# Kernel tuning notes

Measured on AMD Instinct MI355X. Metric: run time of the kernel, lower is better.

The kernel has to match this reference:

```python
import jax, jax.numpy as jnp
import numpy as np

# Constants from retinanet.settings (repo defaults, undefined in snippet; fixed here)
ALPHA = 0.95
GAMMA = 2.0
DAMPENING = 0.7           # DAMPENING_PARAMETER; gt_map simplified to all-False
MAX_POS_DIST = 30.0       # MAX_ANOT_ANCHOR_POSITION_DISTANCE
MAX_ANG_DIST = 20.0       # MAX_ANOT_ANCHOR_ANGLE_DISTANCE
EPS = 1e-4


def setup_inputs() -> dict:
    key = jax.random.key(0)
    k1, k2, k3, k4, k5 = jax.random.split(key, 5)
    B, N, K, C = 4, 300000, 64, 4
    classifications = jax.random.uniform(k1, (B, N, C), jnp.float32, 0.01, 0.99)
    regressions = jax.random.normal(k2, (B, N, 3), jnp.float32) * 5.0
    anchors = jax.random.uniform(k3, (B, N, 3), jnp.float32) * jnp.array([512.0, 512.0, 180.0])
    ann_xy_a = jax.random.uniform(k4, (B, K, 3), jnp.float32) * jnp.array([512.0, 512.0, 180.0])
    ann_cls = jax.random.randint(k5, (B, K, 1), 0, C).astype(jnp.float32)
    annotations = jnp.concatenate([ann_xy_a, ann_cls], axis=-1)  # [B,K,4]
    return {"classifications": classifications, "regressions": regressions,
            "anchors": anchors, "annotations": annotations}


def _per_image(classification, regression, ann, anchor):
    C = classification.shape[1]
    cls = jnp.clip(classification, EPS, 1.0 - EPS)
    # NxK broadcast distance matrices (the tile/transpose chain in the original)
    dx = jnp.abs(anchor[:, 0, None] - ann[None, :, 0])
    dy = jnp.abs(anchor[:, 1, None] - ann[None, :, 1])
    dalpha = jnp.abs(anchor[:, 2, None] - ann[None, :, 2])
    dxy = jnp.sqrt(dx * dx + dy * dy)                         # [N,K]
    dxy_min = jnp.min(dxy, axis=1)                            # [N]
    dxy_argmin = jnp.argmin(dxy, axis=1)                      # [N]
    a = jnp.take_along_axis(dalpha, dxy_argmin[:, None], axis=1)[:, 0]
    # target assignment
    neg = (dxy_min >= 1.5 * MAX_POS_DIST) | (a >= 1.5 * MAX_ANG_DIST)
    pos = (dxy_min < MAX_POS_DIST) & (a < MAX_ANG_DIST)
    assigned = ann[dxy_argmin]                                # [N,4] gather
    targets = jnp.full(cls.shape, -1.0, cls.dtype)
    targets = jnp.where(neg[:, None], 0.0, targets)
    targets = jnp.where(pos[:, None], 0.0, targets)
    onehot = jax.nn.one_hot(assigned[:, 3].astype(jnp.int32), C, dtype=cls.dtype)
    targets = jnp.where(pos[:, None] & (onehot > 0), 1.0, targets)
    num_pos = jnp.sum(pos).astype(cls.dtype)
    denom = jnp.maximum(num_pos, 1.0)
    # focal-weighted BCE
    alpha_factor = jnp.where(targets == 1.0, ALPHA, 1.0 - ALPHA)
    focal_weight = alpha_factor * jnp.where(targets == 1.0, 1.0 - cls, cls) ** GAMMA
    bce = -(targets * jnp.log(cls) + (1.0 - targets) * jnp.log(1.0 - cls))
    cls_loss = jnp.where(targets != -1.0, focal_weight * bce, 0.0) * DAMPENING
    cls_total = jnp.sum(cls_loss) / denom
    t = assigned[:, :3] - anchor
    diff_xy = jnp.abs(t[:, :2] - regression[:, :2])
    loss_xy = jnp.where(diff_xy <= 1.0 / 9.0, 0.5 * 9.0 * diff_xy ** 2, diff_xy - 0.5 / 9.0) * DAMPENING
    diff_ang = jnp.maximum((jnp.abs(t[:, 2] - regression[:, 2]) - 10.0) / 5.0, 0.0) * DAMPENING
    has_pos = num_pos > 0
    xy_mean = jnp.where(has_pos, jnp.sum(loss_xy * pos[:, None]) / (2.0 * denom), 0.0)
    ang_mean = jnp.where(has_pos, jnp.sum(diff_ang * pos) / denom, 0.0)
    return cls_total, xy_mean, ang_mean


def reference(classifications, regressions, anchors, annotations):
    anchor = anchors[0]  # original uses anchors[0,:,:] for all batch elements
    cls_l, xy_l, ang_l = jax.vmap(lambda c, r, an: _per_image(c, r, an, anchor))(
        classifications, regressions, annotations)
    return jnp.stack([jnp.mean(cls_l), jnp.mean(xy_l), jnp.mean(ang_l)])
```

## Files before the change

### kernel.cpp

```cpp
#include <hip/hip_runtime.h>
#include <cmath>

constexpr int Bk = 4;
constexpr int Nk = 300000;
constexpr int Kk = 64;
constexpr int BLOCK = 256;
constexpr int CHUNK = 4;
constexpr int SUPER = BLOCK * CHUNK;
constexpr int PBI = (Nk + SUPER - 1) / SUPER;
constexpr int NBLK = Bk * PBI;

#define C_ALPHA 0.95f
#define C_DAMP 0.7f


__global__ __launch_bounds__(BLOCK) void focal_main(
    const float* __restrict__ cls_,
    const float* __restrict__ reg_,
    const float* __restrict__ anc_,
    const float* __restrict__ ann_,
    float4* __restrict__ part)
{
    __shared__ float2 s_xy[Kk];
    __shared__ float  s_an[Kk];
    __shared__ float  s_cl[Kk];

    const int b   = blockIdx.x / PBI;
    const int blk = blockIdx.x - b * PBI;
    const int n0  = blk * SUPER + threadIdx.x;

    if (threadIdx.x < Kk) {
        const float4 a4 = reinterpret_cast<const float4*>(ann_)[b * Kk + threadIdx.x];
        s_xy[threadIdx.x] = make_float2(a4.x, a4.y);
        s_an[threadIdx.x] = a4.z;
        s_cl[threadIdx.x] = a4.w;
    }
    __syncthreads();

    int   n[CHUNK];
    bool  val[CHUNK];
    float ax[CHUNK], ay[CHUNK], aa[CHUNK];
    float best[CHUNK];
    int   arg[CHUNK];
    #pragma unroll
    for (int c = 0; c < CHUNK; ++c) {
        n[c]   = n0 + c * BLOCK;
        val[c] = n[c] < Nk;
        const size_t base = (size_t)(val[c] ? n[c] : 0) * 3;
        ax[c] = anc_[base + 0];
        ay[c] = anc_[base + 1];
        aa[c] = anc_[base + 2];
        best[c] = 3.4e38f;
        arg[c]  = 0;
    }

    #pragma unroll
    for (int k = 0; k < Kk; ++k) {
        const float2 axy = s_xy[k];
        #pragma unroll
        for (int c = 0; c < CHUNK; ++c) {
            const float dx = ax[c] - axy.x;
            const float dy = ay[c] - axy.y;
            const float d  = fmaf(dy, dy, dx * dx);
            if (d < best[c]) { best[c] = d; arg[c] = k; }
        }
    }

    float cls_sum = 0.f, xy_sum = 0.f, ang_sum = 0.f, posn = 0.f;

    #pragma unroll
    for (int c = 0; c < CHUNK; ++c) {
        if (!val[c]) continue;
        const int   a    = arg[c];
        const float aang = fabsf(aa[c] - s_an[a]);
        const bool  posm = (best[c] < 900.0f)  && (aang < 20.0f);
        const bool  negm = (best[c] >= 2025.0f) || (aang >= 30.0f);
        posn += posm ? 1.0f : 0.0f;

        if (posm || negm) {
            const int cidx = (int)s_cl[a];
            const float4 p4 = reinterpret_cast<const float4*>(cls_)[(size_t)b * Nk + n[c]];
            const float p[4] = {p4.x, p4.y, p4.z, p4.w};
            float s = 0.f;
            #pragma unroll
            for (int cc = 0; cc < 4; ++cc) {
                const float pc  = fminf(fmaxf(p[cc], 1e-4f), 1.0f - 1e-4f);
                const bool  t1  = posm && (cc == cidx);
                const float af  = t1 ? C_ALPHA : (1.0f - C_ALPHA);
                const float w   = t1 ? (1.0f - pc) : pc;
                const float bce = t1 ? (-__logf(pc)) : (-__logf(1.0f - pc));
                s += af * w * w * bce;
            }
            cls_sum += s * C_DAMP;
        }

        if (posm) {
            const size_t rb = ((size_t)b * Nk + n[c]) * 3;
            const float rx = reg_[rb + 0];
            const float ry = reg_[rb + 1];
            const float ra = reg_[rb + 2];
            const float tx = s_xy[a].x - ax[c];
            const float ty = s_xy[a].y - ay[c];
            const float ta = s_an[a]   - aa[c];
            const float d0 = fabsf(tx - rx);
            const float d1 = fabsf(ty - ry);
            const float l0 = (d0 <= (1.0f / 9.0f)) ? 4.5f * d0 * d0 : d0 - (0.5f / 9.0f);
            const float l1 = (d1 <= (1.0f / 9.0f)) ? 4.5f * d1 * d1 : d1 - (0.5f / 9.0f);
            xy_sum += (l0 + l1) * C_DAMP;
            ang_sum += fmaxf((fabsf(ta - ra) - 10.0f) / 5.0f, 0.0f) * C_DAMP;
        }
    }

    #pragma unroll
    for (int off = 32; off > 0; off >>= 1) {
        cls_sum += __shfl_down(cls_sum, off, 64);
        xy_sum  += __shfl_down(xy_sum,  off, 64);
        ang_sum += __shfl_down(ang_sum, off, 64);
        posn    += __shfl_down(posn,    off, 64);
    }
    __shared__ float r0[4], r1[4], r2[4], r3[4];
    const int wave = threadIdx.x >> 6;
    const int lane = threadIdx.x & 63;
    if (lane == 0) { r0[wave] = cls_sum; r1[wave] = xy_sum; r2[wave] = ang_sum; r3[wave] = posn; }
    __syncthreads();
    if (threadIdx.x == 0) {
        part[blockIdx.x] = make_float4(r0[0] + r0[1] + r0[2] + r0[3],
                                       r1[0] + r1[1] + r1[2] + r1[3],
                                       r2[0] + r2[1] + r2[2] + r2[3],
                                       r3[0] + r3[1] + r3[2] + r3[3]);
    }
}

__global__ __launch_bounds__(256) void focal_finalize(
    const float4* __restrict__ part, float* __restrict__ out)
{
    const int b    = threadIdx.x >> 6;
    const int lane = threadIdx.x & 63;
    double c = 0.0, x = 0.0, g = 0.0, q = 0.0;
    for (int i = lane; i < PBI; i += 64) {
        const float4 p = part[b * PBI + i];
        c += (double)p.x; x += (double)p.y; g += (double)p.z; q += (double)p.w;
    }
    #pragma unroll
    for (int off = 32; off > 0; off >>= 1) {
        c += __shfl_down(c, off, 64);
        x += __shfl_down(x, off, 64);
        g += __shfl_down(g, off, 64);
        q += __shfl_down(q, off, 64);
    }
    __shared__ double sc[4], sx[4], sg[4], sq[4];
    if (lane == 0) { sc[b] = c; sx[b] = x; sg[b] = g; sq[b] = q; }
    __syncthreads();
    if (threadIdx.x == 0) {
        double cm = 0.0, xm = 0.0, am = 0.0;
        for (int bb = 0; bb < Bk; ++bb) {
            const double np_   = sq[bb];
            const double denom = np_ > 1.0 ? np_ : 1.0;
            cm += sc[bb] / denom;
            if (np_ > 0.0) {
                xm += sx[bb] / (2.0 * denom);
                am += sg[bb] / denom;
            }
        }
        out[0] = (float)(cm / (double)Bk);
        out[1] = (float)(xm / (double)Bk);
        out[2] = (float)(am / (double)Bk);
    }
}

extern "C" void kernel_launch(void* const* d_in, const int* in_sizes, int n_in,
                              void* d_out, int out_size, void* d_ws, size_t ws_size,
                              hipStream_t stream)
{
    const float* cls_ = (const float*)d_in[0];
    const float* reg_ = (const float*)d_in[1];
    const float* anc_ = (const float*)d_in[2];
    const float* ann_ = (const float*)d_in[3];
    float4* part = (float4*)d_ws;

    focal_main<<<dim3(NBLK), dim3(BLOCK), 0, stream>>>(cls_, reg_, anc_, ann_, part);
    focal_finalize<<<dim3(1), dim3(256), 0, stream>>>(part, (float*)d_out);
}
```

Before: 102.2 us.

## Vectorize anchor loads, prefetch classifications, and compute focal loss branch-free

Each thread now owns four consecutive anchors, so it loads the anchor triples as three float4 reads and prefetches its four classification float4s before the 64-annotation distance loop. The classification loss is computed unconditionally as a negative-target base sum, plus a correction for the assigned class on positive anchors. This removes the divergent conditional loads and branches and lets the memory latency overlap the compute loop. In exchange, every anchor now pays for the loads and logs even when it is ignored, and register use rises.

```diff
diff --git a/kernel.cpp b/kernel.cpp
--- a/kernel.cpp
+++ b/kernel.cpp
@@ -11,6 +11,7 @@
 constexpr int NBLK = Bk * PBI;
 
 #define C_ALPHA 0.95f
+#define C_NALPHA (1.0f - 0.95f)
 #define C_DAMP 0.7f
 
 
@@ -27,32 +28,60 @@
 
     const int b   = blockIdx.x / PBI;
     const int blk = blockIdx.x - b * PBI;
-    const int n0  = blk * SUPER + threadIdx.x;
-
-    if (threadIdx.x < Kk) {
-        const float4 a4 = reinterpret_cast<const float4*>(ann_)[b * Kk + threadIdx.x];
-        s_xy[threadIdx.x] = make_float2(a4.x, a4.y);
-        s_an[threadIdx.x] = a4.z;
-        s_cl[threadIdx.x] = a4.w;
+    const int tid = threadIdx.x;
+    const int a0  = blk * SUPER + tid * CHUNK;
+
+    if (tid < Kk) {
+        const float4 a4 = reinterpret_cast<const float4*>(ann_)[b * Kk + tid];
+        s_xy[tid] = make_float2(a4.x, a4.y);
+        s_an[tid] = a4.z;
+        s_cl[tid] = a4.w;
     }
     __syncthreads();
 
-    int   n[CHUNK];
-    bool  val[CHUNK];
+    const bool full = (a0 + CHUNK) <= Nk;
+
     float ax[CHUNK], ay[CHUNK], aa[CHUNK];
+    if (full) {
+        const float4* a4p = reinterpret_cast<const float4*>(anc_);
+        const int fb = 3 * (blk * BLOCK + tid);
+        const float4 r0 = a4p[fb + 0];
+        const float4 r1 = a4p[fb + 1];
+        const float4 r2 = a4p[fb + 2];
+        ax[0] = r0.x; ay[0] = r0.y; aa[0] = r0.z;
+        ax[1] = r0.w; ay[1] = r1.x; aa[1] = r1.y;
+        ax[2] = r1.z; ay[2] = r1.w; aa[2] = r2.x;
+        ax[3] = r2.y; ay[3] = r2.z; aa[3] = r2.w;
+    } else {
+        #pragma unroll
+        for (int c = 0; c < CHUNK; ++c) {
+            const int n = a0 + c;
+            if (n < Nk) {
+                ax[c] = anc_[(size_t)n * 3 + 0];
+                ay[c] = anc_[(size_t)n * 3 + 1];
+                aa[c] = anc_[(size_t)n * 3 + 2];
+            } else { ax[c] = 1e9f; ay[c] = 1e9f; aa[c] = 0.f; }
+        }
+    }
+
+    float4 p4[CHUNK];
+    if (full) {
+        const float4* c4 = reinterpret_cast<const float4*>(cls_) + (size_t)b * Nk + a0;
+        #pragma unroll
+        for (int c = 0; c < CHUNK; ++c) p4[c] = c4[c];
+    } else {
+        #pragma unroll
+        for (int c = 0; c < CHUNK; ++c) {
+            const int n = a0 + c;
+            p4[c] = (n < Nk) ? reinterpret_cast<const float4*>(cls_)[(size_t)b * Nk + n]
+                             : make_float4(0.5f, 0.5f, 0.5f, 0.5f);
+        }
+    }
+
     float best[CHUNK];
     int   arg[CHUNK];
     #pragma unroll
-    for (int c = 0; c < CHUNK; ++c) {
-        n[c]   = n0 + c * BLOCK;
-        val[c] = n[c] < Nk;
-        const size_t base = (size_t)(val[c] ? n[c] : 0) * 3;
-        ax[c] = anc_[base + 0];
-        ay[c] = anc_[base + 1];
-        aa[c] = anc_[base + 2];
-        best[c] = 3.4e38f;
-        arg[c]  = 0;
-    }
+    for (int c = 0; c < CHUNK; ++c) { best[c] = 3.4e38f; arg[c] = 0; }
 
     #pragma unroll
     for (int k = 0; k < Kk; ++k) {
@@ -70,32 +99,34 @@
 
     #pragma unroll
     for (int c = 0; c < CHUNK; ++c) {
-        if (!val[c]) continue;
-        const int   a    = arg[c];
-        const float aang = fabsf(aa[c] - s_an[a]);
-        const bool  posm = (best[c] < 900.0f)  && (aang < 20.0f);
-        const bool  negm = (best[c] >= 2025.0f) || (aang >= 30.0f);
+        const bool  valid = full || (a0 + c < Nk);
+        const int   a     = arg[c];
+        const float aang  = fabsf(aa[c] - s_an[a]);
+        const bool  posm  = valid && (best[c] < 900.0f)   && (aang < 20.0f);
+        const bool  negm  = valid && ((best[c] >= 2025.0f) || (aang >= 30.0f));
         posn += posm ? 1.0f : 0.0f;
 
-        if (posm || negm) {
+        const float p[4] = {p4[c].x, p4[c].y, p4[c].z, p4[c].w};
+        float base = 0.f;
+        #pragma unroll
+        for (int cc = 0; cc < 4; ++cc) {
+            const float pc = fminf(fmaxf(p[cc], 1e-4f), 1.0f - 1e-4f);
+            base = fmaf(pc * pc, -__logf(1.0f - pc), base);
+        }
+        float s = C_NALPHA * base;
+        if (posm) {
             const int cidx = (int)s_cl[a];
-            const float4 p4 = reinterpret_cast<const float4*>(cls_)[(size_t)b * Nk + n[c]];
-            const float p[4] = {p4.x, p4.y, p4.z, p4.w};
-            float s = 0.f;
-            #pragma unroll
-            for (int cc = 0; cc < 4; ++cc) {
-                const float pc  = fminf(fmaxf(p[cc], 1e-4f), 1.0f - 1e-4f);
-                const bool  t1  = posm && (cc == cidx);
-                const float af  = t1 ? C_ALPHA : (1.0f - C_ALPHA);
-                const float w   = t1 ? (1.0f - pc) : pc;
-                const float bce = t1 ? (-__logf(pc)) : (-__logf(1.0f - pc));
-                s += af * w * w * bce;
-            }
-            cls_sum += s * C_DAMP;
-        }
+            float pc = (cidx < 2) ? (cidx == 0 ? p[0] : p[1])
+                                  : (cidx == 2 ? p[2] : p[3]);
+            pc = fminf(fmaxf(pc, 1e-4f), 1.0f - 1e-4f);
+            s -= C_NALPHA * pc * pc * (-__logf(1.0f - pc));
+            const float q = 1.0f - pc;
+            s += C_ALPHA * q * q * (-__logf(pc));
+        }
+        cls_sum += (posm || negm) ? s * C_DAMP : 0.f;
 
         if (posm) {
-            const size_t rb = ((size_t)b * Nk + n[c]) * 3;
+            const size_t rb = ((size_t)b * Nk + (a0 + c)) * 3;
             const float rx = reg_[rb + 0];
             const float ry = reg_[rb + 1];
             const float ra = reg_[rb + 2];
@@ -118,16 +149,16 @@
         ang_sum += __shfl_down(ang_sum, off, 64);
         posn    += __shfl_down(posn,    off, 64);
     }
-    __shared__ float r0[4], r1[4], r2[4], r3[4];
-    const int wave = threadIdx.x >> 6;
-    const int lane = threadIdx.x & 63;
-    if (lane == 0) { r0[wave] = cls_sum; r1[wave] = xy_sum; r2[wave] = ang_sum; r3[wave] = posn; }
+    __shared__ float r0s[4], r1s[4], r2s[4], r3s[4];
+    const int wave = tid >> 6;
+    const int lane = tid & 63;
+    if (lane == 0) { r0s[wave] = cls_sum; r1s[wave] = xy_sum; r2s[wave] = ang_sum; r3s[wave] = posn; }
     __syncthreads();
-    if (threadIdx.x == 0) {
-        part[blockIdx.x] = make_float4(r0[0] + r0[1] + r0[2] + r0[3],
-                                       r1[0] + r1[1] + r1[2] + r1[3],
-                                       r2[0] + r2[1] + r2[2] + r2[3],
-                                       r3[0] + r3[1] + r3[2] + r3[3]);
+    if (tid == 0) {
+        part[blockIdx.x] = make_float4(r0s[0] + r0s[1] + r0s[2] + r0s[3],
+                                       r1s[0] + r1s[1] + r1s[2] + r1s[3],
+                                       r2s[0] + r2s[1] + r2s[2] + r2s[3],
+                                       r3s[0] + r3s[1] + r3s[2] + r3s[3]);
     }
 }
 
```

Result: no change. 102.2 us (+0.1%).
